# Performance work log

Hardware: AMD Instinct MI355X
Metric: run time of the kernel (lower is better)

Reference implementation:

```python
import jax, jax.numpy as jnp
import numpy as np

B, CIN, COUT, H, W = 8, 128, 128, 64, 64

# kernel-grid base offsets (dy, dx), row-major k = kh*3 + kw, matching torch base_offset-1
BASE = jnp.array([[-1, -1], [-1, 0], [-1, 1],
                  [0, -1], [0, 0], [0, 1],
                  [1, -1], [1, 0], [1, 1]], dtype=jnp.float32)  # [9,2]
CORNER = jnp.array([1, 0, 1, 0, 0, 0, 1, 0, 1], dtype=jnp.float32)  # mask1 per kernel tap
EDGE = jnp.array([0, 1, 0, 1, 0, 1, 0, 1, 0], dtype=jnp.float32)    # mask2 per kernel tap


def conv3x3(x, w, b=None):
    out = jax.lax.conv_general_dilated(
        x, w, window_strides=(1, 1), padding=((1, 1), (1, 1)),
        dimension_numbers=('NCHW', 'OIHW', 'NCHW'))
    if b is not None:
        out = out + b[None, :, None, None]
    return out


def bilinear_sample(x, py, px):
    Bv, C, Hin, Win = x.shape
    y0 = jnp.floor(py)
    x0 = jnp.floor(px)
    wy = py - y0
    wx = px - x0
    y0i = y0.astype(jnp.int32)
    x0i = x0.astype(jnp.int32)
    xf = x.reshape(Bv, C, Hin * Win)

    def corner(yi, xi):
        valid = ((yi >= 0) & (yi < Hin) & (xi >= 0) & (xi < Win)).astype(x.dtype)
        idx = jnp.clip(yi, 0, Hin - 1) * Win + jnp.clip(xi, 0, Win - 1)  # [B,K,Ho,Wo]
        g = jax.vmap(lambda xb, ib: xb[:, ib])(xf, idx)  # [B,C,K,Ho,Wo]
        return g * valid[:, None]

    v00 = corner(y0i, x0i)
    v01 = corner(y0i, x0i + 1)
    v10 = corner(y0i + 1, x0i)
    v11 = corner(y0i + 1, x0i + 1)
    wy = wy[:, None]
    wx = wx[:, None]
    return (v00 * (1 - wy) * (1 - wx) + v01 * (1 - wy) * wx
            + v10 * wy * (1 - wx) + v11 * wy * wx)


def setup_inputs() -> dict:
    key = jax.random.key(0)
    k1, k2, k3 = jax.random.split(key, 3)
    x = jax.random.normal(k1, (B, CIN, H, W), dtype=jnp.float32)
    # small offset-conv weights keep predicted offsets in a realistic sub-pixel range
    w_off = jax.random.normal(k2, (5, CIN, 3, 3), dtype=jnp.float32) * 0.02
    b_off = jnp.zeros((5,), dtype=jnp.float32)
    w = jax.random.normal(k3, (COUT, CIN, 3, 3), dtype=jnp.float32) * (1.0 / np.sqrt(CIN * 9))
    b = jnp.zeros((COUT,), dtype=jnp.float32)
    return {"x": x, "w_off": w_off, "b_off": b_off, "w": w, "b": b}


def reference(x, w_off, b_off, w, b):
    off = conv3x3(x, w_off, b_off)          # [B,5,H,W]
    scale1 = jax.nn.relu(off[:, 2:3]) + 1.0  # corner scale [B,1,H,W]
    scale2 = jax.nn.relu(off[:, 3:4]) + 1.0  # edge scale   [B,1,H,W]
    shift = off[:, :2]                       # equivariant shift vector [B,2,H,W]

    # per-tap scale; center tap gets 0 but its base offset is (0,0) anyway
    scale_k = CORNER[None, :, None, None] * scale1 + EDGE[None, :, None, None] * scale2  # [B,9,H,W]
    # deform offset = scaled_base - base + shift = base*(scale-1) + shift
    delta = BASE[None, :, :, None, None] * (scale_k - 1.0)[:, :, None] + shift[:, None]  # [B,9,2,H,W]

    hs = jnp.arange(H, dtype=x.dtype)
    ws = jnp.arange(W, dtype=x.dtype)
    # sampling positions: p0 + base_k + offset_k (stride=1, pad=1)
    py = hs[None, None, :, None] + BASE[None, :, 0, None, None] + delta[:, :, 0]  # [B,9,H,W]
    px = ws[None, None, None, :] + BASE[None, :, 1, None, None] + delta[:, :, 1]

    sampled = bilinear_sample(x, py, px)  # [B,CIN,9,H,W]
    out = jnp.einsum('bckhw,ock->bohw', sampled, w.reshape(COUT, CIN, 9))
    return out + b[None, :, None, None]
```

## Files before the change

### kernel.cpp

```cpp
#include <hip/hip_runtime.h>

#define Wd 64
#define Hd 64
#define HWp 4096
#define CIN_ 128
#define COUT_ 128

typedef __bf16 bf16x8 __attribute__((ext_vector_type(8)));
typedef float f32x4 __attribute__((ext_vector_type(4)));

__device__ inline ushort f2bf(float f) {
    unsigned u = __float_as_uint(f);
    u += 0x7fff + ((u >> 16) & 1);
    return (ushort)(u >> 16);
}
__device__ inline float bflo(unsigned u) { return __uint_as_float(u << 16); }
__device__ inline float bfhi(unsigned u) { return __uint_as_float(u & 0xffff0000u); }
__device__ inline unsigned bfround(float f) {
    unsigned u = __float_as_uint(f);
    return u + 0x7fff + ((u >> 16) & 1);
}
__device__ inline unsigned pack2(float lo, float hi) {
    return __builtin_amdgcn_perm(bfround(hi), bfround(lo), 0x07060302);
}

__global__ __launch_bounds__(256) void prep_kernel(
    const float* __restrict__ x, const float* __restrict__ w,
    const float* __restrict__ w_off, ushort* __restrict__ xt,
    ushort* __restrict__ w_t, float* __restrict__ wr)
{
    __shared__ ushort tile[128 * 136];
    int blk = blockIdx.x;
    int t = threadIdx.x;

    if (blk < 256) {
        int b = blk >> 5, yx0 = (blk & 31) << 7;
        const float* xb = x + (size_t)b * CIN_ * HWp + yx0;
        int lanelo = t & 31, grp = t >> 5;
        #pragma unroll
        for (int i = 0; i < 4; i++) {
            int cbase = i * 32 + grp * 4;
            float4 v0 = *(const float4*)(xb + (size_t)(cbase + 0) * HWp + lanelo * 4);
            float4 v1 = *(const float4*)(xb + (size_t)(cbase + 1) * HWp + lanelo * 4);
            float4 v2 = *(const float4*)(xb + (size_t)(cbase + 2) * HWp + lanelo * 4);
            float4 v3 = *(const float4*)(xb + (size_t)(cbase + 3) * HWp + lanelo * 4);
            ushort4 u;
            u.x = f2bf(v0.x); u.y = f2bf(v1.x); u.z = f2bf(v2.x); u.w = f2bf(v3.x);
            *(ushort4*)&tile[(lanelo * 4 + 0) * 136 + cbase] = u;
            u.x = f2bf(v0.y); u.y = f2bf(v1.y); u.z = f2bf(v2.y); u.w = f2bf(v3.y);
            *(ushort4*)&tile[(lanelo * 4 + 1) * 136 + cbase] = u;
            u.x = f2bf(v0.z); u.y = f2bf(v1.z); u.z = f2bf(v2.z); u.w = f2bf(v3.z);
            *(ushort4*)&tile[(lanelo * 4 + 2) * 136 + cbase] = u;
            u.x = f2bf(v0.w); u.y = f2bf(v1.w); u.z = f2bf(v2.w); u.w = f2bf(v3.w);
            *(ushort4*)&tile[(lanelo * 4 + 3) * 136 + cbase] = u;
        }
        __syncthreads();
        ushort* dst = xt + ((size_t)b * HWp + yx0) * CIN_;
        int c8 = (t & 15) * 8, yxg = t >> 4;
        #pragma unroll
        for (int i = 0; i < 8; i++) {
            int yxl = i * 16 + yxg;
            int4 v = *(int4*)&tile[yxl * 136 + c8];
            *(int4*)(dst + (size_t)yxl * CIN_ + c8) = v;
        }
    } else if (blk < 832) {
        int i = (blk - 256) * 256 + t;
        int ci = i & 31, o = (i >> 5) & 127, s = i >> 12;
        int k = s >> 2, q = s & 3, c = q * 32 + ci;
        w_t[i] = f2bf(w[o * 1152 + c * 9 + k]);
    } else {
        int i = (blk - 832) * 256 + t;
        if (i < 4608) {
            int j = i & 3, r = i >> 2;
            int tap = r % 9, c = r / 9;
            wr[c * 36 + tap * 4 + j] = w_off[j * 1152 + c * 9 + tap];
        }
    }
}

__global__ __launch_bounds__(256, 2) void offsets_kernel(
    const float* __restrict__ x, const float* __restrict__ wr,
    const float* __restrict__ b_off, int4* __restrict__ midx,
    float4* __restrict__ mw)
{
    __shared__ float wl[4608];
    __shared__ float part[256 * 4];
    __shared__ float der[64 * 4];

    int t = threadIdx.x;
    int b = blockIdx.x >> 6;
    int h = blockIdx.x & 63;

    for (int i = t; i < 4608; i += 256) wl[i] = wr[i];
    __syncthreads();

    int pi = t & 63, cc = t >> 6;
    const float* xb = x + (size_t)(b * CIN_ + cc * 32) * HWp;

    int idx9[9];
    float msk9[9];
    #pragma unroll
    for (int dy = 0; dy < 3; dy++) {
        int hy = h + dy - 1;
        int hyc = min(max(hy, 0), Hd - 1);
        bool vr = (hy >= 0) && (hy < Hd);
        #pragma unroll
        for (int dx = 0; dx < 3; dx++) {
            int wx = pi + dx - 1;
            int wxc = min(max(wx, 0), Wd - 1);
            bool v = vr && (wx >= 0) && (wx < Wd);
            idx9[dy * 3 + dx] = hyc * Wd + wxc;
            msk9[dy * 3 + dx] = v ? 1.0f : 0.0f;
        }
    }

    float o0 = 0.f, o1 = 0.f, o2 = 0.f, o3 = 0.f;
    #pragma unroll 2
    for (int c = 0; c < 32; c++) {
        const float* xp = xb + c * HWp;
        const float* wc = &wl[(cc * 32 + c) * 36];
        float xv[9];
        #pragma unroll
        for (int tp = 0; tp < 9; tp++) xv[tp] = xp[idx9[tp]] * msk9[tp];
        #pragma unroll
        for (int tp = 0; tp < 9; tp++) {
            float4 wj = *(const float4*)&wc[tp * 4];
            o0 += xv[tp] * wj.x; o1 += xv[tp] * wj.y;
            o2 += xv[tp] * wj.z; o3 += xv[tp] * wj.w;
        }
    }
    part[t * 4 + 0] = o0;
    part[t * 4 + 1] = o1;
    part[t * 4 + 2] = o2;
    part[t * 4 + 3] = o3;
    __syncthreads();

    if (t < 64) {
        float s0 = b_off[0], s1 = b_off[1], s2 = b_off[2], s3 = b_off[3];
        #pragma unroll
        for (int q = 0; q < 4; q++) {
            s0 += part[(q * 64 + t) * 4 + 0];
            s1 += part[(q * 64 + t) * 4 + 1];
            s2 += part[(q * 64 + t) * 4 + 2];
            s3 += part[(q * 64 + t) * 4 + 3];
        }
        der[t * 4 + 0] = s0;
        der[t * 4 + 1] = s1;
        der[t * 4 + 2] = fmaxf(s2, 0.f) + 1.f;
        der[t * 4 + 3] = fmaxf(s3, 0.f) + 1.f;
    }
    __syncthreads();

    #pragma unroll
    for (int s = 0; s < 3; s++) {
        int q = t + s * 256;
        if (q < 576) {
            int k = q >> 6;
            int pp = q & 63;
            float sy = der[pp * 4 + 0], sx = der[pp * 4 + 1];
            float sc1 = der[pp * 4 + 2], sc2 = der[pp * 4 + 3];
            int ky = k / 3, kx = k - ky * 3;
            float by = (float)(ky - 1), bx = (float)(kx - 1);
            bool corner = (ky != 1) && (kx != 1);
            bool edge = (ky != 1) ^ (kx != 1);
            float sk = corner ? sc1 : (edge ? sc2 : 0.0f);
            float py = (float)h + by * sk + sy;
            float px = (float)pp + bx * sk + sx;
            float y0f = floorf(py), x0f = floorf(px);
            float wy = py - y0f, wx = px - x0f;
            int y0 = (int)y0f, x0 = (int)x0f;
            int y1 = y0 + 1, x1 = x0 + 1;
            float vy0 = (y0 >= 0 && y0 < Hd) ? 1.f : 0.f;
            float vy1 = (y1 >= 0 && y1 < Hd) ? 1.f : 0.f;
            float vx0 = (x0 >= 0 && x0 < Wd) ? 1.f : 0.f;
            float vx1 = (x1 >= 0 && x1 < Wd) ? 1.f : 0.f;
            int cy0 = min(max(y0, 0), Hd - 1), cy1 = min(max(y1, 0), Hd - 1);
            int cx0 = min(max(x0, 0), Wd - 1), cx1 = min(max(x1, 0), Wd - 1);
            int4 ii;
            ii.x = cy0 * Wd + cx0;
            ii.y = cy0 * Wd + cx1;
            ii.z = cy1 * Wd + cx0;
            ii.w = cy1 * Wd + cx1;
            float4 ww;
            ww.x = (1.f - wy) * (1.f - wx) * vy0 * vx0;
            ww.y = (1.f - wy) * wx * vy0 * vx1;
            ww.z = wy * (1.f - wx) * vy1 * vx0;
            ww.w = wy * wx * vy1 * vx1;
            int addr = (b * 9 + k) * HWp + h * Wd + pp;
            midx[addr] = ii;
            mw[addr] = ww;
        }
    }
}

struct Gath { int4 g0, g1, g2, g3, wa; };

__global__ __launch_bounds__(512, 2) void deform_gemm_mfma(
    const ushort* __restrict__ xt, const ushort* __restrict__ w_t,
    const float* __restrict__ bias, const int4* __restrict__ midx,
    const float4* __restrict__ mw, float* __restrict__ out)
{
    __shared__ ushort A_lds[2][128 * 40];
    __shared__ ushort S_lds[2][128 * 40];

    int t = threadIdx.x;
    int b = blockIdx.x >> 5;
    int rp = blockIdx.x & 31;
    int p0 = rp << 7;
    const ushort* xtb = xt + (size_t)b * HWp * CIN_;

    int p = t >> 2;
    int c8 = (t & 3) << 3;

    int wv = t >> 6, lane = t & 63;
    int wm = wv & 1, wn = wv >> 1;
    int lm = lane & 15, lq = lane >> 4;

    f32x4 acc[4][2] = {};

    int4 mi = midx[(b * 9 + 0) * HWp + p0 + p];
    float4 mv = mw[(b * 9 + 0) * HWp + p0 + p];

    auto issue = [&](int s) -> Gath {
        int q = s & 3;
        const ushort* base = xtb + q * 32 + c8;
        Gath r;
        r.g0 = *(const int4*)(base + mi.x * CIN_);
        r.g1 = *(const int4*)(base + mi.y * CIN_);
        r.g2 = *(const int4*)(base + mi.z * CIN_);
        r.g3 = *(const int4*)(base + mi.w * CIN_);
        r.wa = *(const int4*)(w_t + s * 4096 + t * 8);
        return r;
    };
    auto commit = [&](int nb, const Gath& G) {
        const unsigned* u0 = (const unsigned*)&G.g0;
        const unsigned* u1 = (const unsigned*)&G.g1;
        const unsigned* u2 = (const unsigned*)&G.g2;
        const unsigned* u3 = (const unsigned*)&G.g3;
        unsigned sd[4];
        #pragma unroll
        for (int d = 0; d < 4; d++) {
            float vlo = mv.x * bflo(u0[d]) + mv.y * bflo(u1[d])
                      + mv.z * bflo(u2[d]) + mv.w * bflo(u3[d]);
            float vhi = mv.x * bfhi(u0[d]) + mv.y * bfhi(u1[d])
                      + mv.z * bfhi(u2[d]) + mv.w * bfhi(u3[d]);
            sd[d] = pack2(vlo, vhi);
        }
        *(int4*)&S_lds[nb][p * 40 + c8] = *(const int4*)sd;
        *(int4*)&A_lds[nb][(t >> 2) * 40 + c8] = G.wa;
    };

    {
        Gath G = issue(0);
        commit(0, G);
    }
    __syncthreads();

    for (int s = 0; s < 36; s++) {
        int cur = s & 1;
        bool prod = (s + 1 < 36);
        Gath Gn;
        if (prod) {
            if (((s + 1) & 3) == 0) {
                int k = (s + 1) >> 2;
                mi = midx[(b * 9 + k) * HWp + p0 + p];
                mv = mw[(b * 9 + k) * HWp + p0 + p];
            }
            Gn = issue(s + 1);
        }

        bf16x8 af[4], bfr[2];
        #pragma unroll
        for (int i = 0; i < 4; i++)
            af[i] = *(const bf16x8*)&A_lds[cur][(wm * 64 + i * 16 + lm) * 40 + lq * 8];
        #pragma unroll
        for (int j = 0; j < 2; j++)
            bfr[j] = *(const bf16x8*)&S_lds[cur][(wn * 32 + j * 16 + lm) * 40 + lq * 8];
        #pragma unroll
        for (int i = 0; i < 4; i++)
            #pragma unroll
            for (int j = 0; j < 2; j++)
                acc[i][j] = __builtin_amdgcn_mfma_f32_16x16x32_bf16(
                    af[i], bfr[j], acc[i][j], 0, 0, 0);

        if (prod) commit(cur ^ 1, Gn);
        __syncthreads();
    }

    #pragma unroll
    for (int i = 0; i < 4; i++) {
        #pragma unroll
        for (int r = 0; r < 4; r++) {
            int o = wm * 64 + i * 16 + lq * 4 + r;
            float bv = bias[o];
            float* orow = out + (size_t)(b * COUT_ + o) * HWp + p0 + wn * 32 + lm;
            #pragma unroll
            for (int j = 0; j < 2; j++)
                orow[j * 16] = acc[i][j][r] + bv;
        }
    }
}

extern "C" void kernel_launch(void* const* d_in, const int* in_sizes, int n_in,
                              void* d_out, int out_size, void* d_ws, size_t ws_size,
                              hipStream_t stream) {
    const float* x     = (const float*)d_in[0];
    const float* w_off = (const float*)d_in[1];
    const float* b_off = (const float*)d_in[2];
    const float* w     = (const float*)d_in[3];
    const float* bias  = (const float*)d_in[4];
    float* out = (float*)d_out;

    char* ws = (char*)d_ws;
    ushort* xt   = (ushort*)ws;
    ushort* w_t  = (ushort*)(ws + 8388608);
    int4*   midx = (int4*)(ws + 8683520);
    float4* mwp  = (float4*)(ws + 13402112);
    float*  wr   = (float*)(ws + 18120704);

    prep_kernel<<<850, 256, 0, stream>>>(x, w, w_off, xt, w_t, wr);
    offsets_kernel<<<512, 256, 0, stream>>>(x, wr, b_off, midx, mwp);
    deform_gemm_mfma<<<256, 512, 0, stream>>>(xt, w_t, bias, midx, mwp, out);
}
```

Baseline: 127.1 us.

## Fuse prep and offsets kernels, load GEMM weights directly into MFMA registers

Merges the prep and offset-conv kernels into a single launch, with the offset weights transposed in shared memory per block instead of through a separate workspace pass. The deform GEMM now uses 256-thread blocks over 64-pixel tiles, 512 blocks in total. It reads the weight operand from a pre-swizzled global layout straight into registers, so the A tile no longer goes through LDS. This removes one launch and the LDS traffic for A, at the cost of redundant global weight loads per wave, more register pressure, and smaller tiles.

```diff
diff --git a/kernel.cpp b/kernel.cpp
--- a/kernel.cpp
+++ b/kernel.cpp
@@ -24,16 +24,18 @@
     return __builtin_amdgcn_perm(bfround(hi), bfround(lo), 0x07060302);
 }
 
-__global__ __launch_bounds__(256) void prep_kernel(
+__global__ __launch_bounds__(256) void prep_offsets_kernel(
     const float* __restrict__ x, const float* __restrict__ w,
-    const float* __restrict__ w_off, ushort* __restrict__ xt,
-    ushort* __restrict__ w_t, float* __restrict__ wr)
+    const float* __restrict__ w_off, const float* __restrict__ b_off,
+    ushort* __restrict__ xt, ushort* __restrict__ w_t2,
+    int4* __restrict__ midx, float4* __restrict__ mw)
 {
-    __shared__ ushort tile[128 * 136];
+    __shared__ char smem[34816];
     int blk = blockIdx.x;
     int t = threadIdx.x;
 
     if (blk < 256) {
+        ushort* tile = (ushort*)smem;
         int b = blk >> 5, yx0 = (blk & 31) << 7;
         const float* xb = x + (size_t)b * CIN_ * HWp + yx0;
         int lanelo = t & 31, grp = t >> 5;
@@ -65,148 +67,143 @@
         }
     } else if (blk < 832) {
         int i = (blk - 256) * 256 + t;
-        int ci = i & 31, o = (i >> 5) & 127, s = i >> 12;
-        int k = s >> 2, q = s & 3, c = q * 32 + ci;
-        w_t[i] = f2bf(w[o * 1152 + c * 9 + k]);
+        int j    = i & 7;
+        int lane = (i >> 3) & 63;
+        int ii   = (i >> 9) & 3;
+        int wm   = (i >> 11) & 1;
+        int s    = i >> 12;
+        int o = wm * 64 + ii * 16 + (lane & 15);
+        int c = (s & 3) * 32 + (lane >> 4) * 8 + j;
+        int k = s >> 2;
+        w_t2[i] = f2bf(w[o * 1152 + c * 9 + k]);
     } else {
-        int i = (blk - 832) * 256 + t;
-        if (i < 4608) {
-            int j = i & 3, r = i >> 2;
-            int tap = r % 9, c = r / 9;
-            wr[c * 36 + tap * 4 + j] = w_off[j * 1152 + c * 9 + tap];
+        float* wl   = (float*)smem;
+        float* part = (float*)(smem + 18432);
+        float* der  = (float*)(smem + 22528);
+        int blk2 = blk - 832;
+        int b = blk2 >> 6;
+        int h = blk2 & 63;
+
+        for (int i = t; i < 4608; i += 256) {
+            int j = i / 1152;
+            int r = i - j * 1152;
+            wl[r * 4 + j] = w_off[i];
+        }
+        __syncthreads();
+
+        int pi = t & 63, cc = t >> 6;
+        const float* xb = x + (size_t)(b * CIN_ + cc * 32) * HWp;
+
+        int idx9[9];
+        float msk9[9];
+        #pragma unroll
+        for (int dy = 0; dy < 3; dy++) {
+            int hy = h + dy - 1;
+            int hyc = min(max(hy, 0), Hd - 1);
+            bool vr = (hy >= 0) && (hy < Hd);
+            #pragma unroll
+            for (int dx = 0; dx < 3; dx++) {
+                int wx = pi + dx - 1;
+                int wxc = min(max(wx, 0), Wd - 1);
+                bool v = vr && (wx >= 0) && (wx < Wd);
+                idx9[dy * 3 + dx] = hyc * Wd + wxc;
+                msk9[dy * 3 + dx] = v ? 1.0f : 0.0f;
+            }
+        }
+
+        float o0 = 0.f, o1 = 0.f, o2 = 0.f, o3 = 0.f;
+        #pragma unroll 2
+        for (int c = 0; c < 32; c++) {
+            const float* xp = xb + c * HWp;
+            const float* wc = &wl[(cc * 32 + c) * 36];
+            float xv[9];
+            #pragma unroll
+            for (int tp = 0; tp < 9; tp++) xv[tp] = xp[idx9[tp]] * msk9[tp];
+            #pragma unroll
+            for (int tp = 0; tp < 9; tp++) {
+                float4 wj = *(const float4*)&wc[tp * 4];
+                o0 += xv[tp] * wj.x; o1 += xv[tp] * wj.y;
+                o2 += xv[tp] * wj.z; o3 += xv[tp] * wj.w;
+            }
+        }
+        part[t * 4 + 0] = o0;
+        part[t * 4 + 1] = o1;
+        part[t * 4 + 2] = o2;
+        part[t * 4 + 3] = o3;
+        __syncthreads();
+
+        if (t < 64) {
+            float s0 = b_off[0], s1 = b_off[1], s2 = b_off[2], s3 = b_off[3];
+            #pragma unroll
+            for (int q = 0; q < 4; q++) {
+                s0 += part[(q * 64 + t) * 4 + 0];
+                s1 += part[(q * 64 + t) * 4 + 1];
+                s2 += part[(q * 64 + t) * 4 + 2];
+                s3 += part[(q * 64 + t) * 4 + 3];
+            }
+            der[t * 4 + 0] = s0;
+            der[t * 4 + 1] = s1;
+            der[t * 4 + 2] = fmaxf(s2, 0.f) + 1.f;
+            der[t * 4 + 3] = fmaxf(s3, 0.f) + 1.f;
+        }
+        __syncthreads();
+
+        #pragma unroll
+        for (int s = 0; s < 3; s++) {
+            int q = t + s * 256;
+            if (q < 576) {
+                int k = q >> 6;
+                int pp = q & 63;
+                float sy = der[pp * 4 + 0], sx = der[pp * 4 + 1];
+                float sc1 = der[pp * 4 + 2], sc2 = der[pp * 4 + 3];
+                int ky = k / 3, kx = k - ky * 3;
+                float by = (float)(ky - 1), bx = (float)(kx - 1);
+                bool corner = (ky != 1) && (kx != 1);
+                bool edge = (ky != 1) ^ (kx != 1);
+                float sk = corner ? sc1 : (edge ? sc2 : 0.0f);
+                float py = (float)h + by * sk + sy;
+                float px = (float)pp + bx * sk + sx;
+                float y0f = floorf(py), x0f = floorf(px);
+                float wy = py - y0f, wx = px - x0f;
+                int y0 = (int)y0f, x0 = (int)x0f;
+                int y1 = y0 + 1, x1 = x0 + 1;
+                float vy0 = (y0 >= 0 && y0 < Hd) ? 1.f : 0.f;
+                float vy1 = (y1 >= 0 && y1 < Hd) ? 1.f : 0.f;
+                float vx0 = (x0 >= 0 && x0 < Wd) ? 1.f : 0.f;
+                float vx1 = (x1 >= 0 && x1 < Wd) ? 1.f : 0.f;
+                int cy0 = min(max(y0, 0), Hd - 1), cy1 = min(max(y1, 0), Hd - 1);
+                int cx0 = min(max(x0, 0), Wd - 1), cx1 = min(max(x1, 0), Wd - 1);
+                int4 ii;
+                ii.x = cy0 * Wd + cx0;
+                ii.y = cy0 * Wd + cx1;
+                ii.z = cy1 * Wd + cx0;
+                ii.w = cy1 * Wd + cx1;
+                float4 ww;
+                ww.x = (1.f - wy) * (1.f - wx) * vy0 * vx0;
+                ww.y = (1.f - wy) * wx * vy0 * vx1;
+                ww.z = wy * (1.f - wx) * vy1 * vx0;
+                ww.w = wy * wx * vy1 * vx1;
+                int addr = (b * 9 + k) * HWp + h * Wd + pp;
+                midx[addr] = ii;
+                mw[addr] = ww;
+            }
         }
     }
 }
 
-__global__ __launch_bounds__(256, 2) void offsets_kernel(
-    const float* __restrict__ x, const float* __restrict__ wr,
-    const float* __restrict__ b_off, int4* __restrict__ midx,
-    float4* __restrict__ mw)
+struct Gath { int4 g0, g1, g2, g3; int4 a0, a1, a2, a3; };
+
+__global__ __launch_bounds__(256, 2) void deform_gemm_mfma(
+    const ushort* __restrict__ xt, const ushort* __restrict__ w_t2,
+    const float* __restrict__ bias, const int4* __restrict__ midx,
+    const float4* __restrict__ mw, float* __restrict__ out)
 {
-    __shared__ float wl[4608];
-    __shared__ float part[256 * 4];
-    __shared__ float der[64 * 4];
+    __shared__ ushort S_lds[2][64 * 40];
 
     int t = threadIdx.x;
     int b = blockIdx.x >> 6;
     int h = blockIdx.x & 63;
-
-    for (int i = t; i < 4608; i += 256) wl[i] = wr[i];
-    __syncthreads();
-
-    int pi = t & 63, cc = t >> 6;
-    const float* xb = x + (size_t)(b * CIN_ + cc * 32) * HWp;
-
-    int idx9[9];
-    float msk9[9];
-    #pragma unroll
-    for (int dy = 0; dy < 3; dy++) {
-        int hy = h + dy - 1;
-        int hyc = min(max(hy, 0), Hd - 1);
-        bool vr = (hy >= 0) && (hy < Hd);
-        #pragma unroll
-        for (int dx = 0; dx < 3; dx++) {
-            int wx = pi + dx - 1;
-            int wxc = min(max(wx, 0), Wd - 1);
-            bool v = vr && (wx >= 0) && (wx < Wd);
-            idx9[dy * 3 + dx] = hyc * Wd + wxc;
-            msk9[dy * 3 + dx] = v ? 1.0f : 0.0f;
-        }
-    }
-
-    float o0 = 0.f, o1 = 0.f, o2 = 0.f, o3 = 0.f;
-    #pragma unroll 2
-    for (int c = 0; c < 32; c++) {
-        const float* xp = xb + c * HWp;
-        const float* wc = &wl[(cc * 32 + c) * 36];
-        float xv[9];
-        #pragma unroll
-        for (int tp = 0; tp < 9; tp++) xv[tp] = xp[idx9[tp]] * msk9[tp];
-        #pragma unroll
-        for (int tp = 0; tp < 9; tp++) {
-            float4 wj = *(const float4*)&wc[tp * 4];
-            o0 += xv[tp] * wj.x; o1 += xv[tp] * wj.y;
-            o2 += xv[tp] * wj.z; o3 += xv[tp] * wj.w;
-        }
-    }
-    part[t * 4 + 0] = o0;
-    part[t * 4 + 1] = o1;
-    part[t * 4 + 2] = o2;
-    part[t * 4 + 3] = o3;
-    __syncthreads();
-
-    if (t < 64) {
-        float s0 = b_off[0], s1 = b_off[1], s2 = b_off[2], s3 = b_off[3];
-        #pragma unroll
-        for (int q = 0; q < 4; q++) {
-            s0 += part[(q * 64 + t) * 4 + 0];
-            s1 += part[(q * 64 + t) * 4 + 1];
-            s2 += part[(q * 64 + t) * 4 + 2];
-            s3 += part[(q * 64 + t) * 4 + 3];
-        }
-        der[t * 4 + 0] = s0;
-        der[t * 4 + 1] = s1;
-        der[t * 4 + 2] = fmaxf(s2, 0.f) + 1.f;
-        der[t * 4 + 3] = fmaxf(s3, 0.f) + 1.f;
-    }
-    __syncthreads();
-
-    #pragma unroll
-    for (int s = 0; s < 3; s++) {
-        int q = t + s * 256;
-        if (q < 576) {
-            int k = q >> 6;
-            int pp = q & 63;
-            float sy = der[pp * 4 + 0], sx = der[pp * 4 + 1];
-            float sc1 = der[pp * 4 + 2], sc2 = der[pp * 4 + 3];
-            int ky = k / 3, kx = k - ky * 3;
-            float by = (float)(ky - 1), bx = (float)(kx - 1);
-            bool corner = (ky != 1) && (kx != 1);
-            bool edge = (ky != 1) ^ (kx != 1);
-            float sk = corner ? sc1 : (edge ? sc2 : 0.0f);
-            float py = (float)h + by * sk + sy;
-            float px = (float)pp + bx * sk + sx;
-            float y0f = floorf(py), x0f = floorf(px);
-            float wy = py - y0f, wx = px - x0f;
-            int y0 = (int)y0f, x0 = (int)x0f;
-            int y1 = y0 + 1, x1 = x0 + 1;
-            float vy0 = (y0 >= 0 && y0 < Hd) ? 1.f : 0.f;
-            float vy1 = (y1 >= 0 && y1 < Hd) ? 1.f : 0.f;
-            float vx0 = (x0 >= 0 && x0 < Wd) ? 1.f : 0.f;
-            float vx1 = (x1 >= 0 && x1 < Wd) ? 1.f : 0.f;
-            int cy0 = min(max(y0, 0), Hd - 1), cy1 = min(max(y1, 0), Hd - 1);
-            int cx0 = min(max(x0, 0), Wd - 1), cx1 = min(max(x1, 0), Wd - 1);
-            int4 ii;
-            ii.x = cy0 * Wd + cx0;
-            ii.y = cy0 * Wd + cx1;
-            ii.z = cy1 * Wd + cx0;
-            ii.w = cy1 * Wd + cx1;
-            float4 ww;
-            ww.x = (1.f - wy) * (1.f - wx) * vy0 * vx0;
-            ww.y = (1.f - wy) * wx * vy0 * vx1;
-            ww.z = wy * (1.f - wx) * vy1 * vx0;
-            ww.w = wy * wx * vy1 * vx1;
-            int addr = (b * 9 + k) * HWp + h * Wd + pp;
-            midx[addr] = ii;
-            mw[addr] = ww;
-        }
-    }
-}
-
-struct Gath { int4 g0, g1, g2, g3, wa; };
-
-__global__ __launch_bounds__(512, 2) void deform_gemm_mfma(
-    const ushort* __restrict__ xt, const ushort* __restrict__ w_t,
-    const float* __restrict__ bias, const int4* __restrict__ midx,
-    const float4* __restrict__ mw, float* __restrict__ out)
-{
-    __shared__ ushort A_lds[2][128 * 40];
-    __shared__ ushort S_lds[2][128 * 40];
-
-    int t = threadIdx.x;
-    int b = blockIdx.x >> 5;
-    int rp = blockIdx.x & 31;
-    int p0 = rp << 7;
+    int p0 = h << 6;
     const ushort* xtb = xt + (size_t)b * HWp * CIN_;
 
     int p = t >> 2;
@@ -229,10 +226,14 @@
         r.g1 = *(const int4*)(base + mi.y * CIN_);
         r.g2 = *(const int4*)(base + mi.z * CIN_);
         r.g3 = *(const int4*)(base + mi.w * CIN_);
-        r.wa = *(const int4*)(w_t + s * 4096 + t * 8);
+        const ushort* ab = w_t2 + (size_t)(((s * 2 + wm) * 4) * 64 + lane) * 8;
+        r.a0 = *(const int4*)(ab);
+        r.a1 = *(const int4*)(ab + 512);
+        r.a2 = *(const int4*)(ab + 1024);
+        r.a3 = *(const int4*)(ab + 1536);
         return r;
     };
-    auto commit = [&](int nb, const Gath& G) {
+    auto commitS = [&](int nb, const Gath& G) {
         const unsigned* u0 = (const unsigned*)&G.g0;
         const unsigned* u1 = (const unsigned*)&G.g1;
         const unsigned* u2 = (const unsigned*)&G.g2;
@@ -247,13 +248,10 @@
             sd[d] = pack2(vlo, vhi);
         }
         *(int4*)&S_lds[nb][p * 40 + c8] = *(const int4*)sd;
-        *(int4*)&A_lds[nb][(t >> 2) * 40 + c8] = G.wa;
     };
 
-    {
-        Gath G = issue(0);
-        commit(0, G);
-    }
+    Gath Gc = issue(0);
+    commitS(0, Gc);
     __syncthreads();
 
     for (int s = 0; s < 36; s++) {
@@ -269,13 +267,15 @@
             Gn = issue(s + 1);
         }
 
-        bf16x8 af[4], bfr[2];
-        #pragma unroll
-        for (int i = 0; i < 4; i++)
-            af[i] = *(const bf16x8*)&A_lds[cur][(wm * 64 + i * 16 + lm) * 40 + lq * 8];
+        bf16x8 bfr[2];
         #pragma unroll
         for (int j = 0; j < 2; j++)
             bfr[j] = *(const bf16x8*)&S_lds[cur][(wn * 32 + j * 16 + lm) * 40 + lq * 8];
+        bf16x8 af[4];
+        af[0] = *(const bf16x8*)&Gc.a0;
+        af[1] = *(const bf16x8*)&Gc.a1;
+        af[2] = *(const bf16x8*)&Gc.a2;
+        af[3] = *(const bf16x8*)&Gc.a3;
         #pragma unroll
         for (int i = 0; i < 4; i++)
             #pragma unroll
@@ -283,7 +283,10 @@
                 acc[i][j] = __builtin_amdgcn_mfma_f32_16x16x32_bf16(
                     af[i], bfr[j], acc[i][j], 0, 0, 0);
 
-        if (prod) commit(cur ^ 1, Gn);
+        if (prod) {
+            commitS(cur ^ 1, Gn);
+            Gc = Gn;
+        }
         __syncthreads();
     }
 
@@ -313,12 +316,11 @@
 
     char* ws = (char*)d_ws;
     ushort* xt   = (ushort*)ws;
-    ushort* w_t  = (ushort*)(ws + 8388608);
+    ushort* w_t2 = (ushort*)(ws + 8388608);
     int4*   midx = (int4*)(ws + 8683520);
     float4* mwp  = (float4*)(ws + 13402112);
-    float*  wr   = (float*)(ws + 18120704);
-
-    prep_kernel<<<850, 256, 0, stream>>>(x, w, w_off, xt, w_t, wr);
-    offsets_kernel<<<512, 256, 0, stream>>>(x, wr, b_off, midx, mwp);
-    deform_gemm_mfma<<<256, 512, 0, stream>>>(xt, w_t, bias, midx, mwp, out);
-}
+
+    prep_offsets_kernel<<<1344, 256, 0, stream>>>(x, w, w_off, b_off,
+                                                  xt, w_t2, midx, mwp);
+    deform_gemm_mfma<<<512, 256, 0, stream>>>(xt, w_t2, bias, midx, mwp, out);
+}
```

Result: slower. 130.2 us (+2.4%).
